# Kernel tuning notes

Measured on AMD Instinct MI355X. Metric: run time of the kernel, lower is better.

The kernel has to match this reference:

```python
import jax, jax.numpy as jnp
import numpy as np

B, C, D, H = 32, 512, 512, 8  # batch, enc_in channels, d_model, num_heads
W = D // H                    # per-head width in frequency domain
BN_EPS = 1e-5


def _lin(k, din, dout):
    # weight stored as [in, out]; apply as x @ W + b (equivalent to torch Linear)
    return jax.random.normal(k, (din, dout), jnp.float32) / np.sqrt(din)


def setup_inputs() -> dict:
    key = jax.random.key(0)
    ks = jax.random.split(key, 16)
    return {
        "x": jax.random.normal(ks[0], (B, C, D), jnp.float32),
        "W_in": _lin(ks[1], D, D), "b_in": jnp.zeros((D,), jnp.float32),
        "W_q": _lin(ks[2], D, D), "b_q": jnp.zeros((D,), jnp.float32),
        "W_k": _lin(ks[3], D, D), "b_k": jnp.zeros((D,), jnp.float32),
        "W_v": _lin(ks[4], D, D), "b_v": jnp.zeros((D,), jnp.float32),
        "temperature": jnp.ones((H, 1), jnp.float32),
        "W1a": _lin(ks[5], D, D), "b1a": jnp.zeros((D,), jnp.float32),
        "bn_gamma": jnp.ones((C,), jnp.float32),
        "bn_beta": jnp.zeros((C,), jnp.float32),
        "bn_mean": 0.1 * jax.random.normal(ks[6], (C,), jnp.float32),
        "bn_var": 1.0 + 0.1 * jax.random.uniform(ks[7], (C,), jnp.float32),
        "W1b": _lin(ks[8], D, D), "b1b": jnp.zeros((D,), jnp.float32),
        "W_out": _lin(ks[9], 2 * D, D), "b_out": jnp.zeros((D,), jnp.float32),
    }


def _complex_l2_normalize(z):
    # torch F.normalize on complex: divide by L2 norm of |z| along last dim
    n = jnp.sqrt(jnp.sum(jnp.abs(z) ** 2, axis=-1, keepdims=True))
    return z / jnp.maximum(n, 1e-12)


def reference(x, W_in, b_in, W_q, b_q, W_k, b_k, W_v, b_v, temperature,
              W1a, b1a, bn_gamma, bn_beta, bn_mean, bn_var, W1b, b1b,
              W_out, b_out):
    b, c, d = x.shape
    h, w = H, d // H

    conv2 = x @ W_in + b_in                       # in_projector (dropout = identity, eval)
    q = conv2 @ W_q + b_q
    k = conv2 @ W_k + b_k
    v = conv2 @ W_v + b_v

    # 2-D FFT over last two axes (c, d), as torch.fft.fft2 does on [b, c, d]
    q_f = jnp.fft.fft2(q).reshape(b, c, h, w)
    k_f = jnp.fft.fft2(k).reshape(b, c, h, w)
    v_f = jnp.fft.fft2(v).reshape(b, c, h, w)
    tep = jnp.fft.fft2(conv2)                     # [b, c, d] complex

    q_f = _complex_l2_normalize(q_f)
    k_f = _complex_l2_normalize(k_f)

    # [b, c, h, h] complex attention scores, scaled by real (8,1) temperature
    attn = jnp.einsum('bchw,bcgw->bchg', q_f, k_f) * temperature
    # custom complex softmax: softmax real and imag parts independently
    attn = jax.nn.softmax(attn.real, axis=-1) + 1j * jax.nn.softmax(attn.imag, axis=-1)

    out_f = jnp.einsum('bchg,bcgw->bchw', attn, v_f)        # complex [b,c,h,w]
    out_f = jnp.abs(jnp.fft.ifft2(out_f)).reshape(b, c, d)  # ifft2 over (h,w)

    # gated branch: Linear -> BatchNorm1d(enc_in, eval) -> ReLU -> Linear -> Sigmoid
    g = tep.real @ W1a + b1a
    g = (g - bn_mean[None, :, None]) * jax.lax.rsqrt(bn_var[None, :, None] + BN_EPS)
    g = g * bn_gamma[None, :, None] + bn_beta[None, :, None]
    g = jax.nn.relu(g) @ W1b + b1b
    g = jax.nn.sigmoid(g)
    out_l = jnp.abs(jnp.fft.ifft2(g * tep))                 # [b, c, d]

    out2 = jnp.concatenate([out_f, out_l], axis=-1) @ W_out + b_out
    return out2 + conv2
```

## Files before the change

kernel.cpp:

```cpp
#include <hip/hip_runtime.h>
#include <hip/hip_bf16.h>

#define FFT_PI 3.14159265358979323846f
#define FOFF(i) ((i) + ((i) >> 3))
#define PR(r) ((r) ^ (((r) >> 3) & 1))

typedef __hip_bfloat16 bf16;
typedef short bf8_t __attribute__((ext_vector_type(8)));
typedef float f4_t __attribute__((ext_vector_type(4)));

__device__ inline float bf2f(unsigned short u) {
    union { unsigned int i; float f; } v; v.i = ((unsigned int)u) << 16; return v.f;
}
__device__ inline unsigned short f2bf(float f) {
    bf16 h = __float2bfloat16(f);
    union { bf16 h; unsigned short u; } v; v.h = h; return v.u;
}
__device__ inline float2 c_load(const ushort2* p) {
    ushort2 u = *p;
    return make_float2(bf2f(u.x), bf2f(u.y));
}
__device__ inline ushort2 c_store(float2 z) {
    ushort2 u; u.x = f2bf(z.x); u.y = f2bf(z.y); return u;
}
__device__ inline int brev6(int t) {
    return ((t & 1) << 5) | ((t & 2) << 3) | ((t & 4) << 1) |
           ((t & 8) >> 1) | ((t & 16) >> 3) | ((t & 32) >> 5);
}
__device__ inline float2 cadd(float2 a, float2 b){ return make_float2(a.x+b.x, a.y+b.y); }
__device__ inline float2 csub(float2 a, float2 b){ return make_float2(a.x-b.x, a.y-b.y); }
__device__ inline float2 cmul(float2 a, float2 b){
    return make_float2(a.x*b.x - a.y*b.y, a.x*b.y + a.y*b.x);
}
__device__ inline float2 cmuli(float2 a, float s){ return make_float2(-s*a.y, s*a.x); }

__device__ inline float2 twd(const float2* TWL, int j, float sign) {
    float2 t = TWL[j];
    return make_float2(t.x, sign * t.y);
}

__device__ inline void async_load16(const void* gp, void* lp) {
    __builtin_amdgcn_global_load_lds(
        (const __attribute__((address_space(1))) void*)gp,
        (__attribute__((address_space(3))) void*)lp, 16, 0, 0);
}

__global__ __launch_bounds__(256) void transpose_cvt_all(
    const float* __restrict__ s0, const float* __restrict__ s1,
    const float* __restrict__ s2, const float* __restrict__ s3,
    const float* __restrict__ s4, const float* __restrict__ s5,
    const float* __restrict__ s6, bf16* __restrict__ Wt)
{
    const int z = blockIdx.z;
    const int R = (z == 6) ? 1024 : 512;
    if (blockIdx.y * 32 >= R) return;
    const float* src = (z == 0) ? s0 : (z == 1) ? s1 : (z == 2) ? s2 :
                       (z == 3) ? s3 : (z == 4) ? s4 : (z == 5) ? s5 : s6;
    bf16* dst = Wt + (long)z * 262144;
    const int C = 512;

    __shared__ float tile[32][33];
    const int bx = blockIdx.x * 32;
    const int by = blockIdx.y * 32;
    const int tx = threadIdx.x, ty = threadIdx.y;
#pragma unroll
    for (int i = 0; i < 32; i += 8)
        tile[ty + i][tx] = src[(long)(by + ty + i) * C + bx + tx];
    __syncthreads();
#pragma unroll
    for (int i = 0; i < 32; i += 8)
        dst[(long)(bx + ty + i) * R + by + tx] = __float2bfloat16(tile[tx][ty + i]);
}

__global__ __launch_bounds__(256) void mfma_gemm(
    const void* __restrict__ Av, const void* __restrict__ Av2,
    int a_type, int lda, int ksplit,
    const bf16* __restrict__ Bt, int ldb,
    const float* __restrict__ bias0, const float* __restrict__ bias1,
    const float* __restrict__ bias2,
    void* __restrict__ C0, void* __restrict__ C1, void* __restrict__ C2,
    int nper, int out_type, int ldc, int K,
    const float* __restrict__ e0, const float* __restrict__ e1,
    const float* __restrict__ e2, const float* __restrict__ e3)
{
    __shared__ short Asub[128 * 32];
    __shared__ short Bsub[128 * 32];

    const int tid = threadIdx.x;
    const int n0 = blockIdx.x * 128;
    const int m0 = blockIdx.y * 128;
    const int l  = tid & 63;
    const int wv = tid >> 6;
    const int wm = wv & 1, wn = wv >> 1;

    f4_t acc[4][4];
#pragma unroll
    for (int i = 0; i < 4; i++)
#pragma unroll
        for (int j = 0; j < 4; j++)
            acc[i][j] = (f4_t)0.f;

    const int crow = l >> 2;
    const int cpc  = (l & 3) * 8;

    for (int k0 = 0; k0 < K; k0 += 32) {
        const void* As = (k0 < ksplit) ? Av : Av2;
        const int kk = (k0 < ksplit) ? k0 : (k0 - ksplit);

        if (a_type == 0) {
#pragma unroll
            for (int c = 0; c < 2; c++) {
                const int chunk = wv * 2 + c;
                const int row = chunk * 16 + crow;
                async_load16((const bf16*)As + (long)(m0 + row) * lda + kk + cpc,
                             &Asub[chunk * 512]);
                async_load16(Bt + (long)(n0 + row) * ldb + k0 + cpc,
                             &Bsub[chunk * 512]);
            }
        } else {
            const int srow = tid >> 2;
            const int sc8  = (tid & 3) * 8;
#pragma unroll
            for (int p = 0; p < 2; p++) {
                const int row = srow + p * 64;
                const float4* src = (const float4*)((const float*)As
                    + (long)(m0 + row) * lda + kk + sc8);
                float4 u0 = src[0], u1 = src[1];
                bf8_t av;
                av[0] = (short)f2bf(u0.x); av[1] = (short)f2bf(u0.y);
                av[2] = (short)f2bf(u0.z); av[3] = (short)f2bf(u0.w);
                av[4] = (short)f2bf(u1.x); av[5] = (short)f2bf(u1.y);
                av[6] = (short)f2bf(u1.z); av[7] = (short)f2bf(u1.w);
                *(bf8_t*)&Asub[row * 32 + sc8] = av;
            }
#pragma unroll
            for (int c = 0; c < 2; c++) {
                const int chunk = wv * 2 + c;
                const int row = chunk * 16 + crow;
                async_load16(Bt + (long)(n0 + row) * ldb + k0 + cpc,
                             &Bsub[chunk * 512]);
            }
        }
        __syncthreads();

        bf8_t a_frag[4], b_frag[4];
        const int ko = (l >> 4) * 8;
        const int lr = l & 15;
#pragma unroll
        for (int fm = 0; fm < 4; fm++)
            a_frag[fm] = *(bf8_t*)&Asub[(wm * 64 + fm * 16 + lr) * 32 + ko];
#pragma unroll
        for (int fn = 0; fn < 4; fn++)
            b_frag[fn] = *(bf8_t*)&Bsub[(wn * 64 + fn * 16 + lr) * 32 + ko];
#pragma unroll
        for (int fm = 0; fm < 4; fm++)
#pragma unroll
            for (int fn = 0; fn < 4; fn++)
                acc[fm][fn] = __builtin_amdgcn_mfma_f32_16x16x32_bf16(
                    b_frag[fn], a_frag[fm], acc[fm][fn], 0, 0, 0);
        __syncthreads();
    }

    const int sel = n0 / nper;
    const int nb  = sel * nper;
    const float* biasl = (sel == 0) ? bias0 : ((sel == 1) ? bias1 : bias2);
    void* Cl = (sel == 0) ? C0 : ((sel == 1) ? C1 : C2);

    const int em = m0 + wm * 64 + (l & 15);
    const int en = n0 + wn * 64 + ((l >> 4) << 2);
#pragma unroll
    for (int fm = 0; fm < 4; fm++) {
        const long m = em + fm * 16;
        float bnm = 0.f, bnr = 1.f, bng = 1.f, bnb = 0.f;
        if (out_type == 3) {
            const int c = (int)(m & 511);
            bnm = e0[c];
            bnr = 1.0f / sqrtf(e1[c] + 1e-5f);
            bng = e2[c];
            bnb = e3[c];
        }
#pragma unroll
        for (int fn = 0; fn < 4; fn++) {
            const int n = en + fn * 16;
            const int nl = n - nb;
            f4_t v = acc[fm][fn];
            if (biasl) {
#pragma unroll
                for (int r = 0; r < 4; r++) v[r] += biasl[nl + r];
            }
            if (out_type == 0) {
                float4 o; o.x = v[0]; o.y = v[1]; o.z = v[2]; o.w = v[3];
                *(float4*)((float*)Cl + m * ldc + nl) = o;
            } else if (out_type == 1) {
                union { unsigned short u[4]; ushort4 q; } o;
#pragma unroll
                for (int r = 0; r < 4; r++) o.u[r] = f2bf(v[r]);
                *(ushort4*)((bf16*)Cl + m * ldc + nl) = o.q;
            } else if (out_type == 2) {
                union { ushort2 u2[4]; uint4 q; } o;
#pragma unroll
                for (int r = 0; r < 4; r++) { o.u2[r].x = f2bf(v[r]); o.u2[r].y = 0; }
                *(uint4*)((ushort2*)Cl + m * ldc + nl) = o.q;
            } else if (out_type == 3) {
                union { unsigned short u[4]; ushort4 q; } o;
#pragma unroll
                for (int r = 0; r < 4; r++)
                    o.u[r] = f2bf(fmaxf((v[r] - bnm) * bnr * bng + bnb, 0.f));
                *(ushort4*)((bf16*)Cl + m * ldc + nl) = o.q;
            } else {
                union { unsigned short u[4]; ushort4 q; } rsd;
                rsd.q = *(const ushort4*)((const unsigned short*)e0 + m * ldc + nl);
                float4 o;
                o.x = v[0] + bf2f(rsd.u[0]);
                o.y = v[1] + bf2f(rsd.u[1]);
                o.z = v[2] + bf2f(rsd.u[2]);
                o.w = v[3] + bf2f(rsd.u[3]);
                *(float4*)((float*)Cl + m * ldc + nl) = o;
            }
        }
    }
}

__device__ inline void dft8(float2* x, float sgn)
{
    const float c45 = 0.70710678118654752f;
    float2 e0, e1, e2, e3, o0, o1, o2, o3;
    {
        float2 u0 = cadd(x[0], x[4]), u1 = csub(x[0], x[4]);
        float2 u2 = cadd(x[2], x[6]), u3 = cmuli(csub(x[2], x[6]), sgn);
        e0 = cadd(u0, u2); e1 = cadd(u1, u3); e2 = csub(u0, u2); e3 = csub(u1, u3);
    }
    {
        float2 u0 = cadd(x[1], x[5]), u1 = csub(x[1], x[5]);
        float2 u2 = cadd(x[3], x[7]), u3 = cmuli(csub(x[3], x[7]), sgn);
        o0 = cadd(u0, u2); o1 = cadd(u1, u3); o2 = csub(u0, u2); o3 = csub(u1, u3);
    }
    const float2 w1 = make_float2(c45, sgn * c45);
    const float2 w3 = make_float2(-c45, sgn * c45);
    o1 = cmul(o1, w1);
    o2 = cmuli(o2, sgn);
    o3 = cmul(o3, w3);
    x[0] = cadd(e0, o0); x[4] = csub(e0, o0);
    x[1] = cadd(e1, o1); x[5] = csub(e1, o1);
    x[2] = cadd(e2, o2); x[6] = csub(e2, o2);
    x[3] = cadd(e3, o3); x[7] = csub(e3, o3);
}

__device__ inline void fft512_r8(float2* bx0, float2* by0, int lane, float sign,
                                 const float2* TWL)
{
    float2* bx = bx0;
    float2* by = by0;
#pragma unroll
    for (int st = 0; st < 3; st++) {
        int n, m, sstr, p, q;
        if (st == 0)      { n = 512; m = 64; sstr = 1;  p = lane;      q = 0; }
        else if (st == 1) { n = 64;  m = 8;  sstr = 8;  p = lane >> 3; q = lane & 7; }
        else              { n = 8;   m = 1;  sstr = 64; p = 0;         q = lane; }
        float2 x[8];
#pragma unroll
        for (int r = 0; r < 8; r++) x[r] = bx[FOFF(q + sstr * (p + r * m))];
        dft8(x, sign);
        if (p) {
            const int step = (st == 0) ? 1 : 8;
#pragma unroll
            for (int k = 1; k < 8; k++)
                x[k] = cmul(x[k], twd(TWL, p * k * step, sign));
        }
#pragma unroll
        for (int k = 0; k < 8; k++) by[FOFF(q + sstr * (8 * p + k))] = x[k];
        __syncthreads();
        float2* t = bx; bx = by; by = t;
    }
}

__device__ inline void twl_fill(float2* TWL, int t, int nthreads)
{
    for (int j = t; j < 512; j += nthreads) {
        float sw, cw;
        __sincosf((2.0f * FFT_PI) * (float)j / 512.0f, &sw, &cw);
        TWL[j] = make_float2(cw, sw);
    }
}

__global__ __launch_bounds__(256) void fft8_rows_all(
    ushort2* __restrict__ qkv, const bf16* __restrict__ conv2,
    ushort2* __restrict__ tb)
{
    __shared__ float2 B0[4][576], B1[4][576];
    __shared__ float2 TWL[512];
    const int buf = blockIdx.x >> 12;
    const int lb  = blockIdx.x & 4095;
    const int li = threadIdx.x >> 6, lane = threadIdx.x & 63;
    const long line = (long)lb * 4 + li;
    twl_fill(TWL, threadIdx.x, 256);

    if (buf < 3) {
        ushort2* s = qkv + (long)buf * 8388608 + line * 512;
        uint4 r0 = *(const uint4*)(s + lane * 8);
        uint4 r1 = *(const uint4*)(s + lane * 8 + 4);
        float2* dst = &B0[li][9 * lane];
        const ushort2* pp = (const ushort2*)&r0;
#pragma unroll
        for (int j = 0; j < 4; j++) dst[j] = c_load(pp + j);
        pp = (const ushort2*)&r1;
#pragma unroll
        for (int j = 0; j < 4; j++) dst[4 + j] = c_load(pp + j);
        __syncthreads();
        fft512_r8(B0[li], B1[li], lane, -1.f, TWL);
        float2* src = &B1[li][9 * lane];
        union { ushort2 u[4]; uint4 q; } o0, o1;
#pragma unroll
        for (int j = 0; j < 4; j++) {
            float2 z = src[j]; o0.u[j].x = f2bf(z.x); o0.u[j].y = f2bf(z.y);
        }
#pragma unroll
        for (int j = 0; j < 4; j++) {
            float2 z = src[4 + j]; o1.u[j].x = f2bf(z.x); o1.u[j].y = f2bf(z.y);
        }
        *(uint4*)(s + lane * 8) = o0.q;
        *(uint4*)(s + lane * 8 + 4) = o1.q;
    } else {
        uint4 raw = *(const uint4*)((const unsigned short*)conv2 + line * 512 + lane * 8);
        const unsigned short* pp = (const unsigned short*)&raw;
        float2* d = &B0[li][9 * lane];
#pragma unroll
        for (int j = 0; j < 8; j++) d[j] = make_float2(bf2f(pp[j]), 0.f);
        __syncthreads();
        fft512_r8(B0[li], B1[li], lane, -1.f, TWL);
        ushort2* s = tb + line * 512;
        float2* src = &B1[li][9 * lane];
        union { ushort2 u[4]; uint4 q; } o0, o1;
#pragma unroll
        for (int j = 0; j < 4; j++) {
            float2 z = src[j]; o0.u[j].x = f2bf(z.x); o0.u[j].y = f2bf(z.y);
        }
#pragma unroll
        for (int j = 0; j < 4; j++) {
            float2 z = src[4 + j]; o1.u[j].x = f2bf(z.x); o1.u[j].y = f2bf(z.y);
        }
        *(uint4*)(s + lane * 8) = o0.q;
        *(uint4*)(s + lane * 8 + 4) = o1.q;
    }
}

__global__ __launch_bounds__(256) void fft8_rows_gated(
    const bf16* __restrict__ g2, ushort2* __restrict__ tep)
{
    __shared__ float2 B0[4][576], B1[4][576];
    __shared__ float2 TWL[512];
    const int li = threadIdx.x >> 6, lane = threadIdx.x & 63;
    const long line = (long)blockIdx.x * 4 + li;
    ushort2* s = tep + line * 512;
    twl_fill(TWL, threadIdx.x, 256);
    {
        uint4 rg = *(const uint4*)((const unsigned short*)g2 + line * 512 + lane * 8);
        uint4 r0 = *(const uint4*)(s + lane * 8);
        uint4 r1 = *(const uint4*)(s + lane * 8 + 4);
        const unsigned short* gp = (const unsigned short*)&rg;
        float2* d = &B0[li][9 * lane];
        const ushort2* pp = (const ushort2*)&r0;
#pragma unroll
        for (int j = 0; j < 4; j++) {
            float sg = 1.0f / (1.0f + __expf(-bf2f(gp[j])));
            float2 z = c_load(pp + j);
            d[j] = make_float2(sg * z.x, sg * z.y);
        }
        pp = (const ushort2*)&r1;
#pragma unroll
        for (int j = 0; j < 4; j++) {
            float sg = 1.0f / (1.0f + __expf(-bf2f(gp[4 + j])));
            float2 z = c_load(pp + j);
            d[4 + j] = make_float2(sg * z.x, sg * z.y);
        }
    }
    __syncthreads();
    fft512_r8(B0[li], B1[li], lane, +1.f, TWL);
    {
        const float sc = 1.0f / 512.0f;
        float2* src = &B1[li][9 * lane];
        union { ushort2 u[4]; uint4 q; } o0, o1;
#pragma unroll
        for (int j = 0; j < 4; j++) {
            float2 z = src[j];
            o0.u[j].x = f2bf(z.x * sc); o0.u[j].y = f2bf(z.y * sc);
        }
#pragma unroll
        for (int j = 0; j < 4; j++) {
            float2 z = src[4 + j];
            o1.u[j].x = f2bf(z.x * sc); o1.u[j].y = f2bf(z.y * sc);
        }
        *(uint4*)(s + lane * 8) = o0.q;
        *(uint4*)(s + lane * 8 + 4) = o1.q;
    }
}

__global__ __launch_bounds__(512) void fft8_cols16_c2c4(
    ushort2* __restrict__ data, bf16* __restrict__ tepReal, float sign)
{
    __shared__ __align__(16) ushort2 Bu[512][16];
    __shared__ float2 TWL[512];
    const int buf = blockIdx.x >> 10;
    const int rem = blockIdx.x & 1023;
    const int b   = rem >> 5;
    const int c0  = (rem & 31) * 16;
    ushort2* base = data + (long)buf * 8388608 + (long)b * 262144 + c0;
    const int t = threadIdx.x;
    const int lr = t >> 2;
    const int lq = t & 3;
    twl_fill(TWL, t, 512);

#pragma unroll
    for (int it = 0; it < 4; it++) {
        const int row = it * 128 + lr;
        uint4 raw = *(const uint4*)(base + (long)row * 512 + lq * 4);
        *(uint4*)&Bu[PR(row)][lq * 4] = raw;
    }
    __syncthreads();

    const int col = t & 15;
    const int rb  = t >> 4;
#pragma unroll
    for (int st = 0; st < 3; st++) {
        int n, m, s;
        if (st == 0)      { n = 512; m = 64; s = 1;  }
        else if (st == 1) { n = 64;  m = 8;  s = 8;  }
        else              { n = 8;   m = 1;  s = 64; }
        const int step = (st == 0) ? 1 : 8;
        float2 x[2][8];
        int ps[2], qs[2];
#pragma unroll
        for (int i = 0; i < 2; i++) {
            const int role = rb + 32 * i;
            int p, q;
            if (st == 0)      { p = role;      q = 0; }
            else if (st == 1) { p = role >> 3; q = role & 7; }
            else              { p = 0;         q = role; }
            ps[i] = p; qs[i] = q;
#pragma unroll
            for (int r = 0; r < 8; r++) {
                const int rr = q + s * (p + r * m);
                x[i][r] = c_load(&Bu[PR(rr)][col]);
            }
        }
        __syncthreads();
#pragma unroll
        for (int i = 0; i < 2; i++) {
            dft8(x[i], sign);
            const int p = ps[i];
            if (p) {
#pragma unroll
                for (int k = 1; k < 8; k++)
                    x[i][k] = cmul(x[i][k], twd(TWL, p * k * step, sign));
            }
#pragma unroll
            for (int k = 0; k < 8; k++) {
                const int rw = qs[i] + s * (8 * p + k);
                Bu[PR(rw)][col] = c_store(x[i][k]);
            }
        }
        __syncthreads();
    }

#pragma unroll
    for (int it = 0; it < 4; it++) {
        const int row = it * 128 + lr;
        union { uint4 q4; unsigned short s[8]; } o;
        o.q4 = *(const uint4*)&Bu[PR(row)][lq * 4];
        *(uint4*)(base + (long)row * 512 + lq * 4) = o.q4;
        if (buf == 3) {
            ushort4 rl;
            rl.x = o.s[0]; rl.y = o.s[2]; rl.z = o.s[4]; rl.w = o.s[6];
            *(ushort4*)(tepReal + (long)b * 262144 + (long)row * 512 + c0 + lq * 4) = rl;
        }
    }
}

__global__ __launch_bounds__(512) void fft8_cols16_abs(
    const ushort2* __restrict__ src, bf16* __restrict__ dst)
{
    __shared__ __align__(16) ushort2 Bu[512][16];
    __shared__ float2 TWL[512];
    const int b  = blockIdx.x >> 5;
    const int c0 = (blockIdx.x & 31) * 16;
    const ushort2* base = src + (long)b * 262144 + c0;
    const int t = threadIdx.x;
    const int lr = t >> 2;
    const int lq = t & 3;
    twl_fill(TWL, t, 512);

#pragma unroll
    for (int it = 0; it < 4; it++) {
        const int row = it * 128 + lr;
        uint4 raw = *(const uint4*)(base + (long)row * 512 + lq * 4);
        *(uint4*)&Bu[PR(row)][lq * 4] = raw;
    }
    __syncthreads();

    const int col = t & 15;
    const int rb  = t >> 4;
#pragma unroll
    for (int st = 0; st < 3; st++) {
        int n, m, s;
        if (st == 0)      { n = 512; m = 64; s = 1;  }
        else if (st == 1) { n = 64;  m = 8;  s = 8;  }
        else              { n = 8;   m = 1;  s = 64; }
        const int step = (st == 0) ? 1 : 8;
        float2 x[2][8];
        int ps[2], qs[2];
#pragma unroll
        for (int i = 0; i < 2; i++) {
            const int role = rb + 32 * i;
            int p, q;
            if (st == 0)      { p = role;      q = 0; }
            else if (st == 1) { p = role >> 3; q = role & 7; }
            else              { p = 0;         q = role; }
            ps[i] = p; qs[i] = q;
#pragma unroll
            for (int r = 0; r < 8; r++) {
                const int rr = q + s * (p + r * m);
                x[i][r] = c_load(&Bu[PR(rr)][col]);
            }
        }
        __syncthreads();
#pragma unroll
        for (int i = 0; i < 2; i++) {
            dft8(x[i], +1.f);
            const int p = ps[i];
            if (p) {
#pragma unroll
                for (int k = 1; k < 8; k++)
                    x[i][k] = cmul(x[i][k], twd(TWL, p * k * step, +1.f));
            }
#pragma unroll
            for (int k = 0; k < 8; k++) {
                const int rw = qs[i] + s * (8 * p + k);
                Bu[PR(rw)][col] = c_store(x[i][k]);
            }
        }
        __syncthreads();
    }

    const float sc = 1.0f / 512.0f;
#pragma unroll
    for (int it = 0; it < 4; it++) {
        const int row = it * 128 + lr;
        union { unsigned short u[4]; ushort4 q4; } o;
#pragma unroll
        for (int j = 0; j < 4; j++) {
            float2 z = c_load(&Bu[PR(row)][lq * 4 + j]);
            o.u[j] = f2bf(sqrtf(z.x * z.x + z.y * z.y) * sc);
        }
        *(ushort4*)(dst + (long)b * 262144 + (long)row * 512 + c0 + lq * 4) = o.q4;
    }
}

__global__ __launch_bounds__(256) void attn_kernel(
    const ushort2* __restrict__ qf, const ushort2* __restrict__ kf,
    const ushort2* __restrict__ vf, const float* __restrict__ temp,
    bf16* __restrict__ out_f)
{
    __shared__ ushort2 QS[4][8][68];
    __shared__ ushort2 KS[4][8][68];
    __shared__ float2 ATT[4][8][9];

    const int li = threadIdx.x >> 6, lane = threadIdx.x & 63;
    const int bc = blockIdx.x * 4 + li;
    const long base = (long)bc * 512;

    {
        const int h1 = lane >> 4, w1 = (lane & 15) * 4;
        uint4 q0 = *(const uint4*)(qf + base + lane * 4);
        uint4 q1 = *(const uint4*)(qf + base + 256 + lane * 4);
        uint4 k0 = *(const uint4*)(kf + base + lane * 4);
        uint4 k1 = *(const uint4*)(kf + base + 256 + lane * 4);
        *(uint4*)&QS[li][h1][w1]     = q0;
        *(uint4*)&QS[li][h1 + 4][w1] = q1;
        *(uint4*)&KS[li][h1][w1]     = k0;
        *(uint4*)&KS[li][h1 + 4][w1] = k1;
    }
    float2 v[8];
#pragma unroll
    for (int h = 0; h < 8; h++)
        v[h] = c_load(vf + base + h * 64 + lane);
    __syncthreads();

    {
        const int h = lane >> 3, g = lane & 7;
        float ar = 0.f, ai = 0.f, nq = 0.f, nk = 0.f;
#pragma unroll
        for (int w = 0; w < 64; w += 4) {
            uint4 qa = *(const uint4*)&QS[li][h][w];
            uint4 kb = *(const uint4*)&KS[li][g][w];
            const unsigned short* qs = (const unsigned short*)&qa;
            const unsigned short* ks = (const unsigned short*)&kb;
#pragma unroll
            for (int j = 0; j < 4; j++) {
                float qx = bf2f(qs[2 * j]), qy = bf2f(qs[2 * j + 1]);
                float kx = bf2f(ks[2 * j]), ky = bf2f(ks[2 * j + 1]);
                ar += qx * kx - qy * ky;
                ai += qx * ky + qy * kx;
                nq += qx * qx + qy * qy;
                nk += kx * kx + ky * ky;
            }
        }
        const float iq = 1.0f / fmaxf(sqrtf(nq), 1e-12f);
        const float ik = 1.0f / fmaxf(sqrtf(nk), 1e-12f);
        const float s = temp[h] * iq * ik;
        ar *= s; ai *= s;
        float mr = ar, mi = ai;
#pragma unroll
        for (int o = 1; o < 8; o <<= 1) {
            mr = fmaxf(mr, __shfl_xor(mr, o, 64));
            mi = fmaxf(mi, __shfl_xor(mi, o, 64));
        }
        float er = __expf(ar - mr), ei = __expf(ai - mi);
        float sr = er, si = ei;
#pragma unroll
        for (int o = 1; o < 8; o <<= 1) {
            sr += __shfl_xor(sr, o, 64);
            si += __shfl_xor(si, o, 64);
        }
        ATT[li][h][g] = make_float2(er / sr, ei / si);
    }
    __syncthreads();

    float2 o[8];
#pragma unroll
    for (int h = 0; h < 8; h++) {
        float orr = 0.f, oi = 0.f;
#pragma unroll
        for (int g = 0; g < 8; g++) {
            float2 a = ATT[li][h][g], b = v[g];
            orr += a.x * b.x - a.y * b.y;
            oi  += a.x * b.y + a.y * b.x;
        }
        o[h] = make_float2(orr, oi);
    }

#pragma unroll
    for (int m = 32; m >= 1; m >>= 1) {
        float ang = (FFT_PI / (float)m) * (float)(lane & (m - 1));
        float sw, cw;
        __sincosf(ang, &sw, &cw);
        const bool low = (lane & m) == 0;
#pragma unroll
        for (int h = 0; h < 8; h++) {
            float px = __shfl_xor(o[h].x, m, 64);
            float py = __shfl_xor(o[h].y, m, 64);
            float nx, ny;
            if (low) {
                nx = o[h].x + px;
                ny = o[h].y + py;
            } else {
                float dx = px - o[h].x;
                float dy = py - o[h].y;
                nx = dx * cw - dy * sw;
                ny = dx * sw + dy * cw;
            }
            o[h].x = nx; o[h].y = ny;
        }
    }
    const int wr = brev6(lane);

    const float r2 = 0.70710678118654752f;
    const float W8x[8] = {1.f,  r2, 0.f, -r2, -1.f, -r2,  0.f,  r2};
    const float W8y[8] = {0.f,  r2, 1.f,  r2,  0.f, -r2, -1.f, -r2};
    unsigned short* stg = (unsigned short*)&QS[li][0][0];
#pragma unroll
    for (int kh = 0; kh < 8; kh++) {
        float sr = 0.f, si = 0.f;
#pragma unroll
        for (int n = 0; n < 8; n++) {
            const int idx = (n * kh) & 7;
            float wx = W8x[idx], wy = W8y[idx];
            sr += o[n].x * wx - o[n].y * wy;
            si += o[n].x * wy + o[n].y * wx;
        }
        stg[kh * 64 + wr] = f2bf(sqrtf(sr * sr + si * si) * (1.0f / 512.0f));
    }
    __syncthreads();
    uint4 ov = *(uint4*)(stg + lane * 8);
    *(uint4*)((unsigned short*)out_f + base + lane * 8) = ov;
}

extern "C" void kernel_launch(void* const* d_in, const int* in_sizes, int n_in,
                              void* d_out, int out_size, void* d_ws, size_t ws_size,
                              hipStream_t stream)
{
    const float* x     = (const float*)d_in[0];
    const float* W_in  = (const float*)d_in[1];
    const float* b_in  = (const float*)d_in[2];
    const float* W_q   = (const float*)d_in[3];
    const float* b_q   = (const float*)d_in[4];
    const float* W_k   = (const float*)d_in[5];
    const float* b_k   = (const float*)d_in[6];
    const float* W_v   = (const float*)d_in[7];
    const float* b_v   = (const float*)d_in[8];
    const float* temp  = (const float*)d_in[9];
    const float* W1a   = (const float*)d_in[10];
    const float* b1a   = (const float*)d_in[11];
    const float* gam   = (const float*)d_in[12];
    const float* bet   = (const float*)d_in[13];
    const float* mea   = (const float*)d_in[14];
    const float* var   = (const float*)d_in[15];
    const float* W1b   = (const float*)d_in[16];
    const float* b1b   = (const float*)d_in[17];
    const float* W_out = (const float*)d_in[18];
    const float* b_out = (const float*)d_in[19];

    char* wsb = (char*)d_ws;
    const long MB = 1024 * 1024;
    bf16*    conv2b  = (bf16*)wsb;
    bf16*    tepReal = (bf16*)(wsb + 16 * MB);
    ushort2* Qb    = (ushort2*)(wsb + 32 * MB);
    ushort2* Kb    = (ushort2*)(wsb + 64 * MB);
    ushort2* Vb    = (ushort2*)(wsb + 96 * MB);
    ushort2* Tb    = (ushort2*)(wsb + 128 * MB);
    bf16*    Wt    = (bf16*)(wsb + 160 * MB);
    bf16* WT_in  = Wt;
    bf16* WT_q   = Wt + 262144;
    bf16* WT_1a  = Wt + 4 * 262144;
    bf16* WT_1b  = Wt + 5 * 262144;
    bf16* WT_out = Wt + 6 * 262144;
    bf16* outF = (bf16*)Qb;
    bf16* g1b  = (bf16*)Kb;
    bf16* outL = (bf16*)Kb;
    bf16* g2b  = (bf16*)Vb;

    const dim3 ggrid(4, 128), gblk(256);
    const int BIG = 1 << 30;
    const int RB = 4096;

    transpose_cvt_all<<<dim3(16, 32, 7), dim3(32, 8), 0, stream>>>(
        W_in, W_q, W_k, W_v, W1a, W1b, W_out, Wt);

    mfma_gemm<<<ggrid, gblk, 0, stream>>>(
        x, x, 1, 512, BIG, WT_in, 512, b_in, nullptr, nullptr,
        conv2b, nullptr, nullptr, BIG, 1, 512, 512,
        nullptr, nullptr, nullptr, nullptr);

    mfma_gemm<<<dim3(12, 128), gblk, 0, stream>>>(
        conv2b, conv2b, 0, 512, BIG, WT_q, 512, b_q, b_k, b_v,
        Qb, Kb, Vb, 512, 2, 512, 512,
        nullptr, nullptr, nullptr, nullptr);

    fft8_rows_all<<<4 * RB, 256, 0, stream>>>(Qb, conv2b, Tb);

    fft8_cols16_c2c4<<<4096, 512, 0, stream>>>(Qb, tepReal, -1.f);

    attn_kernel<<<RB, 256, 0, stream>>>(Qb, Kb, Vb, temp, outF);

    mfma_gemm<<<ggrid, gblk, 0, stream>>>(
        tepReal, tepReal, 0, 512, BIG, WT_1a, 512, b1a, nullptr, nullptr,
        g1b, nullptr, nullptr, BIG, 3, 512, 512,
        mea, var, gam, bet);

    mfma_gemm<<<ggrid, gblk, 0, stream>>>(
        g1b, g1b, 0, 512, BIG, WT_1b, 512, b1b, nullptr, nullptr,
        g2b, nullptr, nullptr, BIG, 1, 512, 512,
        nullptr, nullptr, nullptr, nullptr);

    fft8_rows_gated<<<RB, 256, 0, stream>>>(g2b, Tb);
    fft8_cols16_abs<<<1024, 512, 0, stream>>>(Tb, outL);

    mfma_gemm<<<ggrid, gblk, 0, stream>>>(
        outF, outL, 0, 512, 512, WT_out, 1024, b_out, nullptr, nullptr,
        d_out, nullptr, nullptr, BIG, 4, 512, 1024,
        (const float*)conv2b, nullptr, nullptr, nullptr);
}
```

Measured before the change: 520.4 us.

## Use bf16 LDS staging in row FFTs, drop intra-wave barriers, table twiddles

The row FFT kernels now keep intermediate stage buffers in shared memory as packed bf16 complex values instead of float2. This halves LDS footprint and traffic, but rounds to bf16 after every radix-8 stage. Block-wide __syncthreads calls inside the FFT stages and in the attention/ifft kernel are removed, relying on each line being owned by a single 64-lane wavefront. The per-stage __sincosf in the in-register ifft is replaced by a small shared twiddle table; added rounding error and the implicit wave-synchronous ordering are the risks.

```diff
diff --git a/kernel.cpp b/kernel.cpp
--- a/kernel.cpp
+++ b/kernel.cpp
@@ -246,11 +246,11 @@
     x[3] = cadd(e3, o3); x[7] = csub(e3, o3);
 }
 
-__device__ inline void fft512_r8(float2* bx0, float2* by0, int lane, float sign,
-                                 const float2* TWL)
-{
-    float2* bx = bx0;
-    float2* by = by0;
+__device__ inline void fft512_r8u(ushort2* bx0, ushort2* by0, int lane, float sign,
+                                  const float2* TWL)
+{
+    ushort2* bx = bx0;
+    ushort2* by = by0;
 #pragma unroll
     for (int st = 0; st < 3; st++) {
         int n, m, sstr, p, q;
@@ -259,7 +259,7 @@
         else              { n = 8;   m = 1;  sstr = 64; p = 0;         q = lane; }
         float2 x[8];
 #pragma unroll
-        for (int r = 0; r < 8; r++) x[r] = bx[FOFF(q + sstr * (p + r * m))];
+        for (int r = 0; r < 8; r++) x[r] = c_load(&bx[FOFF(q + sstr * (p + r * m))]);
         dft8(x, sign);
         if (p) {
             const int step = (st == 0) ? 1 : 8;
@@ -268,9 +268,8 @@
                 x[k] = cmul(x[k], twd(TWL, p * k * step, sign));
         }
 #pragma unroll
-        for (int k = 0; k < 8; k++) by[FOFF(q + sstr * (8 * p + k))] = x[k];
-        __syncthreads();
-        float2* t = bx; bx = by; by = t;
+        for (int k = 0; k < 8; k++) by[FOFF(q + sstr * (8 * p + k))] = c_store(x[k]);
+        ushort2* t = bx; bx = by; by = t;
     }
 }
 
@@ -287,7 +286,7 @@
     ushort2* __restrict__ qkv, const bf16* __restrict__ conv2,
     ushort2* __restrict__ tb)
 {
-    __shared__ float2 B0[4][576], B1[4][576];
+    __shared__ ushort2 B0[4][576], B1[4][576];
     __shared__ float2 TWL[512];
     const int buf = blockIdx.x >> 12;
     const int lb  = blockIdx.x & 4095;
@@ -299,46 +298,38 @@
         ushort2* s = qkv + (long)buf * 8388608 + line * 512;
         uint4 r0 = *(const uint4*)(s + lane * 8);
         uint4 r1 = *(const uint4*)(s + lane * 8 + 4);
-        float2* dst = &B0[li][9 * lane];
+        ushort2* dst = &B0[li][9 * lane];
         const ushort2* pp = (const ushort2*)&r0;
 #pragma unroll
-        for (int j = 0; j < 4; j++) dst[j] = c_load(pp + j);
+        for (int j = 0; j < 4; j++) dst[j] = pp[j];
         pp = (const ushort2*)&r1;
 #pragma unroll
-        for (int j = 0; j < 4; j++) dst[4 + j] = c_load(pp + j);
+        for (int j = 0; j < 4; j++) dst[4 + j] = pp[j];
         __syncthreads();
-        fft512_r8(B0[li], B1[li], lane, -1.f, TWL);
-        float2* src = &B1[li][9 * lane];
+        fft512_r8u(B0[li], B1[li], lane, -1.f, TWL);
+        ushort2* src = &B1[li][9 * lane];
         union { ushort2 u[4]; uint4 q; } o0, o1;
 #pragma unroll
-        for (int j = 0; j < 4; j++) {
-            float2 z = src[j]; o0.u[j].x = f2bf(z.x); o0.u[j].y = f2bf(z.y);
-        }
-#pragma unroll
-        for (int j = 0; j < 4; j++) {
-            float2 z = src[4 + j]; o1.u[j].x = f2bf(z.x); o1.u[j].y = f2bf(z.y);
-        }
+        for (int j = 0; j < 4; j++) o0.u[j] = src[j];
+#pragma unroll
+        for (int j = 0; j < 4; j++) o1.u[j] = src[4 + j];
         *(uint4*)(s + lane * 8) = o0.q;
         *(uint4*)(s + lane * 8 + 4) = o1.q;
     } else {
         uint4 raw = *(const uint4*)((const unsigned short*)conv2 + line * 512 + lane * 8);
         const unsigned short* pp = (const unsigned short*)&raw;
-        float2* d = &B0[li][9 * lane];
-#pragma unroll
-        for (int j = 0; j < 8; j++) d[j] = make_float2(bf2f(pp[j]), 0.f);
+        ushort2* d = &B0[li][9 * lane];
+#pragma unroll
+        for (int j = 0; j < 8; j++) { ushort2 u; u.x = pp[j]; u.y = 0; d[j] = u; }
         __syncthreads();
-        fft512_r8(B0[li], B1[li], lane, -1.f, TWL);
+        fft512_r8u(B0[li], B1[li], lane, -1.f, TWL);
         ushort2* s = tb + line * 512;
-        float2* src = &B1[li][9 * lane];
+        ushort2* src = &B1[li][9 * lane];
         union { ushort2 u[4]; uint4 q; } o0, o1;
 #pragma unroll
-        for (int j = 0; j < 4; j++) {
-            float2 z = src[j]; o0.u[j].x = f2bf(z.x); o0.u[j].y = f2bf(z.y);
-        }
-#pragma unroll
-        for (int j = 0; j < 4; j++) {
-            float2 z = src[4 + j]; o1.u[j].x = f2bf(z.x); o1.u[j].y = f2bf(z.y);
-        }
+        for (int j = 0; j < 4; j++) o0.u[j] = src[j];
+#pragma unroll
+        for (int j = 0; j < 4; j++) o1.u[j] = src[4 + j];
         *(uint4*)(s + lane * 8) = o0.q;
         *(uint4*)(s + lane * 8 + 4) = o1.q;
     }
@@ -347,7 +338,7 @@
 __global__ __launch_bounds__(256) void fft8_rows_gated(
     const bf16* __restrict__ g2, ushort2* __restrict__ tep)
 {
-    __shared__ float2 B0[4][576], B1[4][576];
+    __shared__ ushort2 B0[4][576], B1[4][576];
     __shared__ float2 TWL[512];
     const int li = threadIdx.x >> 6, lane = threadIdx.x & 63;
     const long line = (long)blockIdx.x * 4 + li;
@@ -358,37 +349,37 @@
         uint4 r0 = *(const uint4*)(s + lane * 8);
         uint4 r1 = *(const uint4*)(s + lane * 8 + 4);
         const unsigned short* gp = (const unsigned short*)&rg;
-        float2* d = &B0[li][9 * lane];
+        ushort2* d = &B0[li][9 * lane];
         const ushort2* pp = (const ushort2*)&r0;
 #pragma unroll
         for (int j = 0; j < 4; j++) {
             float sg = 1.0f / (1.0f + __expf(-bf2f(gp[j])));
             float2 z = c_load(pp + j);
-            d[j] = make_float2(sg * z.x, sg * z.y);
+            d[j] = c_store(make_float2(sg * z.x, sg * z.y));
         }
         pp = (const ushort2*)&r1;
 #pragma unroll
         for (int j = 0; j < 4; j++) {
             float sg = 1.0f / (1.0f + __expf(-bf2f(gp[4 + j])));
             float2 z = c_load(pp + j);
-            d[4 + j] = make_float2(sg * z.x, sg * z.y);
+            d[4 + j] = c_store(make_float2(sg * z.x, sg * z.y));
         }
     }
     __syncthreads();
-    fft512_r8(B0[li], B1[li], lane, +1.f, TWL);
+    fft512_r8u(B0[li], B1[li], lane, +1.f, TWL);
     {
         const float sc = 1.0f / 512.0f;
-        float2* src = &B1[li][9 * lane];
+        ushort2* src = &B1[li][9 * lane];
         union { ushort2 u[4]; uint4 q; } o0, o1;
 #pragma unroll
         for (int j = 0; j < 4; j++) {
-            float2 z = src[j];
-            o0.u[j].x = f2bf(z.x * sc); o0.u[j].y = f2bf(z.y * sc);
+            float2 z = c_load(&src[j]);
+            o0.u[j] = c_store(make_float2(z.x * sc, z.y * sc));
         }
 #pragma unroll
         for (int j = 0; j < 4; j++) {
-            float2 z = src[4 + j];
-            o1.u[j].x = f2bf(z.x * sc); o1.u[j].y = f2bf(z.y * sc);
+            float2 z = c_load(&src[4 + j]);
+            o1.u[j] = c_store(make_float2(z.x * sc, z.y * sc));
         }
         *(uint4*)(s + lane * 8) = o0.q;
         *(uint4*)(s + lane * 8 + 4) = o1.q;
@@ -563,10 +554,17 @@
     __shared__ ushort2 QS[4][8][68];
     __shared__ ushort2 KS[4][8][68];
     __shared__ float2 ATT[4][8][9];
+    __shared__ float2 TW32[32];
 
     const int li = threadIdx.x >> 6, lane = threadIdx.x & 63;
     const int bc = blockIdx.x * 4 + li;
     const long base = (long)bc * 512;
+
+    if (lane < 32) {
+        float sw, cw;
+        __sincosf((FFT_PI / 32.0f) * (float)lane, &sw, &cw);
+        TW32[lane] = make_float2(cw, sw);
+    }
 
     {
         const int h1 = lane >> 4, w1 = (lane & 15) * 4;
@@ -583,7 +581,6 @@
 #pragma unroll
     for (int h = 0; h < 8; h++)
         v[h] = c_load(vf + base + h * 64 + lane);
-    __syncthreads();
 
     {
         const int h = lane >> 3, g = lane & 7;
@@ -623,7 +620,6 @@
         }
         ATT[li][h][g] = make_float2(er / sr, ei / si);
     }
-    __syncthreads();
 
     float2 o[8];
 #pragma unroll
@@ -640,9 +636,9 @@
 
 #pragma unroll
     for (int m = 32; m >= 1; m >>= 1) {
-        float ang = (FFT_PI / (float)m) * (float)(lane & (m - 1));
-        float sw, cw;
-        __sincosf(ang, &sw, &cw);
+        const int j = (lane & (m - 1)) * (32 / m);
+        float2 wv = TW32[j];
+        const float cw = wv.x, sw = wv.y;
         const bool low = (lane & m) == 0;
 #pragma unroll
         for (int h = 0; h < 8; h++) {
@@ -679,7 +675,6 @@
         }
         stg[kh * 64 + wr] = f2bf(sqrtf(sr * sr + si * si) * (1.0f / 512.0f));
     }
-    __syncthreads();
     uint4 ov = *(uint4*)(stg + lane * 8);
     *(uint4*)((unsigned short*)out_f + base + lane * 8) = ov;
 }
```

New measurement: 519.8 us. No clear change (-0.1%).
